# Performance work log

Measured on AMD Instinct MI355X. Metric: run time of the kernel, lower is better.

## Reference

```python
import jax, jax.numpy as jnp
import numpy as np

# Model constants (match init_kwargs)
H, P, N, G, NL, K = 32, 64, 128, 1, 15, 4   # heads, head_dim, state, groups, lambda levels, conv width
HID, T, BATCH = 1024, 1024, 1
INTER = H * P                    # 2048
CONV_DIM = INTER + 2 * G * N     # 2304
PROJ = INTER + CONV_DIM + H * (NL + 1)  # 4864
EPS = 1e-5


def _level_matrix(t_len: int) -> np.ndarray:
    """Fenwick-tree level assignment: for query t, prefix [0,t] splits into
    power-of-two segments from binary expansion of t+1; segment of length 2^l -> level l."""
    lm = np.zeros((t_len, t_len), dtype=np.int32)
    for t in range(t_len):
        n = t + 1
        while n > 0:
            lb = n & (-n)
            lm[t, n - lb:n] = lb.bit_length() - 1
            n -= lb
    return lm


def setup_inputs() -> dict:
    key = jax.random.key(0)
    ks = jax.random.split(key, 4)
    return {
        "hidden_states": jax.random.normal(ks[0], (BATCH, T, HID), jnp.float32),
        "in_proj_w": jax.random.normal(ks[1], (PROJ, HID), jnp.float32) / np.sqrt(HID).astype(np.float32),
        "in_proj_b": jnp.zeros((PROJ,), jnp.float32),
        "conv_w": jax.random.normal(ks[2], (CONV_DIM, K), jnp.float32) / np.sqrt(K).astype(np.float32),
        "dt_bias": jnp.ones((H,), jnp.float32),
        "A_log": jnp.log(jnp.arange(1, H + 1, dtype=jnp.float32)),
        "L_param": jnp.ones((H, NL), jnp.float32),
        "D": jnp.ones((H,), jnp.float32),
        "rmsnorm_w": jnp.ones((INTER,), jnp.float32),
        "out_proj_w": jax.random.normal(ks[3], (HID, INTER), jnp.float32) / np.sqrt(INTER).astype(np.float32),
        "out_proj_b": jnp.zeros((HID,), jnp.float32),
        "level_mat": jnp.asarray(_level_matrix(T)),  # (T,T) int32, data-independent
    }


def reference(hidden_states, in_proj_w, in_proj_b, conv_w, dt_bias, A_log,
              L_param, D, rmsnorm_w, out_proj_w, out_proj_b, level_mat):
    b, t, _ = hidden_states.shape
    # in_proj and split: [z | xBC | dt | dl]
    zxbcdtdl = hidden_states @ in_proj_w.T + in_proj_b
    z, xBC, dt, dl = jnp.split(zxbcdtdl, [INTER, INTER + CONV_DIM, INTER + CONV_DIM + H], axis=-1)
    # depthwise causal conv1d (width K) + SiLU
    xp = jnp.pad(xBC, ((0, 0), (K - 1, 0), (0, 0)))
    conv = sum(xp[:, w:w + t, :] * conv_w[:, w] for w in range(K))
    xBC = jax.nn.silu(conv)
    x, Bm, Cm = jnp.split(xBC, [INTER, INTER + G * N], axis=-1)
    x = x.reshape(b, t, H, P)          # v pre-scale
    Bm = Bm.reshape(b, t, G, N)        # keys
    Cm = Cm.reshape(b, t, G, N)        # queries
    dl = dl.reshape(b, t, H, NL)
    # D residual uses unscaled x (matches hmamba_chunk_scan_combined ordering)
    D_res = x * D[None, None, :, None]
    dt = jax.nn.softplus(dt + dt_bias)            # (b,t,H)
    v = x * dt[..., None]                          # (b,t,H,P)
    A = -jnp.exp(A_log)                            # (H,)
    g = A * dt                                     # (b,t,H), per-token log-decay (<=0)
    Ls = jax.nn.softplus(L_param * dl)             # (b,t,H,NL) per-token level scales
    # cumulative log-decay; decay(t,s) = exp(cg_t - cg_s), s<=t
    cg = jnp.cumsum(g, axis=1).transpose(0, 2, 1)  # (b,H,t)
    mask = jnp.tril(jnp.ones((t, t), bool))
    logdecay = jnp.where(mask, cg[:, :, :, None] - cg[:, :, None, :], -jnp.inf)
    decay = jnp.exp(logdecay)                      # (b,H,t,s)
    # hierarchical level scale H[t,s] = Ls[b,t,h, level(t,s)]
    Hmat = jnp.take_along_axis(Ls.transpose(0, 2, 1, 3), level_mat[None, None, :, :], axis=-1)  # (b,H,t,s)
    scores = jnp.einsum('btgn,bsgn->bgts', Cm, Bm)  # (b,G,t,s), G=1 broadcasts over heads
    att = scores * decay * Hmat                     # (b,H,t,s), masked via decay=0
    y = jnp.einsum('bhts,bshp->bthp', att, v) + D_res
    y = y.reshape(b, t, INTER)
    # gated RMSNorm with norm_before_gate=False: normalize(y * silu(z)) * w
    yg = y * jax.nn.silu(z)
    y = yg * jax.lax.rsqrt(jnp.mean(yg * yg, axis=-1, keepdims=True) + EPS) * rmsnorm_w
    return y @ out_proj_w.T + out_proj_b
```

## Files before the change

kernel.cpp:

```cpp
#include <hip/hip_runtime.h>
#include <hip/hip_bf16.h>
#include <math.h>

#define T_LEN 1024
#define HID 1024
#define NHEAD 32
#define HDIM 64
#define NSTATE 128
#define NLVL 15
#define KCONV 4
#define INTER 2048
#define CONV_DIM 2304
#define PROJ 4864
#define EPS 1e-5f

typedef __attribute__((ext_vector_type(8))) _Float16 half8;
typedef __attribute__((ext_vector_type(4))) float float4v;
typedef unsigned short ushort_t;

__device__ __forceinline__ float softplus_f(float x) {
  return fmaxf(x, 0.f) + log1pf(expf(-fabsf(x)));
}
__device__ __forceinline__ float silu_f(float x) {
  return x / (1.f + expf(-x));
}
__device__ __forceinline__ ushort_t f2h(float f) {
  union { _Float16 h; ushort_t u; } v;
  v.h = (_Float16)f;
  return v.u;
}
__device__ __forceinline__ float h2f(ushort_t u) {
  union { ushort_t u; _Float16 h; } v;
  v.u = u;
  return (float)v.h;
}
__device__ __forceinline__ void gload_lds16(const void* g, void* l) {
  __builtin_amdgcn_global_load_lds(
      (const __attribute__((address_space(1))) void*)g,
      (__attribute__((address_space(3))) void*)l, 16, 0, 0);
}

#define N4_HS  (T_LEN * HID / 4)
#define N4_WI  (PROJ * HID / 4)
#define N4_WO  (HID * INTER / 4)
__global__ __launch_bounds__(256) void prep_f16(
    const float* __restrict__ hs, const float* __restrict__ wi,
    const float* __restrict__ wo, ushort_t* __restrict__ hsb,
    ushort_t* __restrict__ wib, ushort_t* __restrict__ wob) {
  int i = blockIdx.x * 256 + threadIdx.x;
  const float* src; ushort_t* dst; int j;
  if (i < N4_HS)              { src = hs; dst = hsb; j = i; }
  else if (i < N4_HS + N4_WI) { src = wi; dst = wib; j = i - N4_HS; }
  else                        { src = wo; dst = wob; j = i - N4_HS - N4_WI; }
  float4 v = reinterpret_cast<const float4*>(src)[j];
  union { ushort_t u[4]; unsigned long long ll; } o;
  o.u[0] = f2h(v.x); o.u[1] = f2h(v.y); o.u[2] = f2h(v.z); o.u[3] = f2h(v.w);
  reinterpret_cast<unsigned long long*>(dst)[j] = o.ll;
}

__global__ __launch_bounds__(256) void gemm_f16_sk(
    const ushort_t* __restrict__ A, const ushort_t* __restrict__ B,
    ushort_t* __restrict__ Cpart, int M, int N, int K, int Kc) {
  __shared__ ushort_t As[2][128][32];
  __shared__ ushort_t Bs[2][128][32];
  const int tid = threadIdx.x;
  const int w = tid >> 6, L = tid & 63;
  const int n0 = blockIdx.x * 128, m0 = blockIdx.y * 128;
  const int kbeg = blockIdx.z * Kc;
  ushort_t* __restrict__ C = Cpart + (size_t)blockIdx.z * M * N;
  const int mq = (w & 1) * 64, nq = (w >> 1) * 64;
  const int srow = (L >> 2);
  const int sch = (L & 3) * 8;

  float4v acc[4][4];
#pragma unroll
  for (int i = 0; i < 4; ++i)
#pragma unroll
    for (int j = 0; j < 4; ++j) acc[i][j] = (float4v){0.f, 0.f, 0.f, 0.f};

  const int niter = Kc / 32;
  {
    const int kk = kbeg;
#pragma unroll
    for (int j = 0; j < 2; ++j) {
      int r0 = 16 * (w * 2 + j);
      gload_lds16(A + (size_t)(m0 + r0 + srow) * K + kk + sch, &As[0][r0][0]);
      gload_lds16(B + (size_t)(n0 + r0 + srow) * K + kk + sch, &Bs[0][r0][0]);
    }
  }
  for (int it = 0; it < niter; ++it) {
    __syncthreads();
    if (it + 1 < niter) {
      const int kk = kbeg + (it + 1) * 32;
      const int nb = (it + 1) & 1;
#pragma unroll
      for (int j = 0; j < 2; ++j) {
        int r0 = 16 * (w * 2 + j);
        gload_lds16(A + (size_t)(m0 + r0 + srow) * K + kk + sch, &As[nb][r0][0]);
        gload_lds16(B + (size_t)(n0 + r0 + srow) * K + kk + sch, &Bs[nb][r0][0]);
      }
    }
    const int cb = it & 1;
    half8 af[4], bf[4];
#pragma unroll
    for (int t = 0; t < 4; ++t) {
      af[t] = *reinterpret_cast<const half8*>(&As[cb][mq + t * 16 + (L & 15)][(L >> 4) * 8]);
      bf[t] = *reinterpret_cast<const half8*>(&Bs[cb][nq + t * 16 + (L & 15)][(L >> 4) * 8]);
    }
#pragma unroll
    for (int mt = 0; mt < 4; ++mt)
#pragma unroll
      for (int nt = 0; nt < 4; ++nt)
        acc[mt][nt] = __builtin_amdgcn_mfma_f32_16x16x32_f16(af[mt], bf[nt], acc[mt][nt], 0, 0, 0);
  }
  const int qrow = (L >> 4) * 4;
#pragma unroll
  for (int mt = 0; mt < 4; ++mt) {
#pragma unroll
    for (int nt = 0; nt < 4; ++nt) {
      int col = n0 + nq + nt * 16 + (L & 15);
#pragma unroll
      for (int r = 0; r < 4; ++r) {
        int row = m0 + mq + mt * 16 + qrow + r;
        C[(size_t)row * N + col] = f2h(acc[mt][nt][r]);
      }
    }
  }
}

__global__ __launch_bounds__(256) void reduce_out4(const ushort_t* __restrict__ p,
                                                   const float* __restrict__ bias,
                                                   float* __restrict__ out, int MN) {
  int i = blockIdx.x * 256 + threadIdx.x;
  if (i * 8 >= MN) return;
  half8 a = reinterpret_cast<const half8*>(p)[i];
  half8 b = reinterpret_cast<const half8*>(p + MN)[i];
  half8 c = reinterpret_cast<const half8*>(p + 2 * (size_t)MN)[i];
  half8 d = reinterpret_cast<const half8*>(p + 3 * (size_t)MN)[i];
  int col = (i * 8) & (HID - 1);
  float o[8];
#pragma unroll
  for (int j = 0; j < 8; ++j)
    o[j] = (float)a[j] + (float)b[j] + (float)c[j] + (float)d[j] + bias[col + j];
  float4 o0 = {o[0], o[1], o[2], o[3]}, o1 = {o[4], o[5], o[6], o[7]};
  reinterpret_cast<float4*>(out)[i * 2] = o0;
  reinterpret_cast<float4*>(out)[i * 2 + 1] = o1;
}

__global__ __launch_bounds__(64) void scan_g(
    const ushort_t* __restrict__ zh0, const ushort_t* __restrict__ zh1,
    const float* __restrict__ in_b, const float* __restrict__ dt_bias,
    const float* __restrict__ A_log, float* __restrict__ dtb,
    double* __restrict__ cgd) {
  const int h = blockIdx.x, l = threadIdx.x;
  const int c = INTER + CONV_DIM + h;
  const float bb = in_b[c] + dt_bias[h];
  const float Ae = -expf(A_log[h]);
  double pre[16];
  double acc = 0.0;
#pragma unroll
  for (int i = 0; i < 16; ++i) {
    int t = l * 16 + i;
    size_t o = (size_t)t * PROJ + c;
    float x = h2f(zh0[o]) + h2f(zh1[o]) + bb;
    float dt = softplus_f(x);
    dtb[t * NHEAD + h] = dt;
    acc += (double)(Ae * dt);
    pre[i] = acc;
  }
  double s = acc;
#pragma unroll
  for (int off = 1; off < 64; off <<= 1) {
    double o = __shfl_up(s, off, 64);
    if (l >= off) s += o;
  }
  const double base = s - acc;
  double* cr = cgd + (size_t)h * T_LEN + l * 16;
#pragma unroll
  for (int i = 0; i < 16; ++i) cr[i] = base + pre[i];
}

__global__ __launch_bounds__(256) void conv_fused(
    const ushort_t* __restrict__ zh0, const ushort_t* __restrict__ zh1,
    const float* __restrict__ in_b, const float* __restrict__ conv_w,
    const float* __restrict__ dtb, const float* __restrict__ Dp,
    ushort_t* __restrict__ vt, float* __restrict__ ybuf,
    ushort_t* __restrict__ Bb, ushort_t* __restrict__ Cb) {
  __shared__ ushort_t Vl[64][68];
  __shared__ float dtl[64];
  const int tq = blockIdx.x, cy = blockIdx.y;
  const int t0 = tq * 64;
  const int tid = threadIdx.x;
  const int lane = tid & 63, g = tid >> 6;
  const bool vpath = (cy < 32);
  const int ccol = vpath ? cy * 64 + lane : INTER + (cy - 32) * 64 + lane;
  const int zcol = INTER + ccol;
  float cw[KCONV];
#pragma unroll
  for (int w = 0; w < KCONV; ++w) cw[w] = conv_w[ccol * KCONV + w];
  const float bc = in_b[zcol];
  if (vpath && tid < 64) dtl[tid] = dtb[(t0 + tid) * NHEAD + cy];
  const float Dh = vpath ? Dp[cy] : 0.f;

  float xv[19];
#pragma unroll
  for (int i = 0; i < 19; ++i) {
    int tt = t0 + g * 16 - 3 + i;
    if (tt >= 0) {
      size_t o = (size_t)tt * PROJ + zcol;
      xv[i] = h2f(zh0[o]) + h2f(zh1[o]) + bc;
    } else xv[i] = 0.f;
  }
  __syncthreads();
#pragma unroll
  for (int i = 0; i < 16; ++i) {
    float acc = xv[i] * cw[0] + xv[i + 1] * cw[1] + xv[i + 2] * cw[2] + xv[i + 3] * cw[3];
    float sil = silu_f(acc);
    int tl = g * 16 + i;
    int t = t0 + tl;
    if (vpath) {
      Vl[tl][lane] = f2h(sil * dtl[tl]);
      ybuf[(size_t)t * INTER + cy * 64 + lane] = sil * Dh;
    } else if (ccol < INTER + NSTATE) {
      Bb[t * NSTATE + (ccol - INTER)] = f2h(sil);
    } else {
      Cb[t * NSTATE + (ccol - INTER - NSTATE)] = f2h(sil);
    }
  }
  if (vpath) {
    __syncthreads();
#pragma unroll
    for (int rep = 0; rep < 2; ++rep) {
      int u = tid + 256 * rep;
      int p = u >> 3, t8 = (u & 7) * 8;
      union { ushort_t u16[8]; half8 h; } o;
#pragma unroll
      for (int j = 0; j < 8; ++j) o.u16[j] = Vl[t8 + j][p];
      *reinterpret_cast<half8*>(vt + (size_t)(cy * 64 + p) * T_LEN + t0 + t8) = o.h;
    }
  }
}

__global__ __launch_bounds__(256) void attn_mfma(
    const ushort_t* __restrict__ Bb, const ushort_t* __restrict__ Cb,
    const ushort_t* __restrict__ vt, const double* __restrict__ cgd,
    const ushort_t* __restrict__ zh0, const ushort_t* __restrict__ zh1,
    const float* __restrict__ in_b, const float* __restrict__ L_param,
    float* __restrict__ ybuf) {
  __shared__ ushort_t Bl[64][136];
  __shared__ ushort_t Vtl[64][72];
  __shared__ ushort_t Sl[64][72];
  __shared__ float Lsl[64][16];
  __shared__ float cgq[64];
  __shared__ float cgs[64];

  const int item = blockIdx.x;
  const int h = item / 40;
  const int rem = item - h * 40;
  int qt, j;
  if (rem < 4)        { qt = rem;                 j = 0; }
  else if (rem < 12)  { qt = 4 + (rem - 4) / 2;   j = (rem - 4) % 2; }
  else if (rem < 24)  { qt = 8 + (rem - 12) / 3;  j = (rem - 12) % 3; }
  else                { qt = 12 + (rem - 24) / 4; j = (rem - 24) % 4; }

  const int tid = threadIdx.x;
  const int w = tid >> 6, L = tid & 63;
  const int tq0 = qt * 64;
  const double* cgh = cgd + (size_t)h * T_LEN;
  const double base = cgh[tq0];

  for (int i = tid; i < 64 * NLVL; i += 256) {
    int r = i / NLVL, l = i - r * NLVL;
    int cc = INTER + CONV_DIM + NHEAD + h * NLVL + l;
    size_t o = (size_t)(tq0 + r) * PROJ + cc;
    float x = h2f(zh0[o]) + h2f(zh1[o]) + in_b[cc];
    Lsl[r][l] = softplus_f(L_param[h * NLVL + l] * x);
  }
  if (tid < 64) cgq[tid] = (float)(cgh[tq0 + tid] - base);

  half8 cfrag[4];
  {
    const ushort_t* cr = Cb + (size_t)(tq0 + w * 16 + (L & 15)) * NSTATE + (L >> 4) * 8;
#pragma unroll
    for (int ks = 0; ks < 4; ++ks)
      cfrag[ks] = *reinterpret_cast<const half8*>(cr + ks * 32);
  }
  float4v yac[4];
#pragma unroll
  for (int i = 0; i < 4; ++i) yac[i] = (float4v){0.f, 0.f, 0.f, 0.f};

  const int qrow = w * 16 + ((L >> 4) << 2);

  const int st0 = 4 * j;
  const int st1 = min(4 * j + 4, qt + 1);
  for (int st = st0; st < st1; ++st) {
    const int ts0 = st * 64;
    __syncthreads();
#pragma unroll
    for (int i = 0; i < 4; ++i) {
      int u = tid + 256 * i;
      int row = u >> 4, kb = (u & 15) * 8;
      *reinterpret_cast<half8*>(&Bl[row][kb]) =
          *reinterpret_cast<const half8*>(Bb + (size_t)(ts0 + row) * NSTATE + kb);
    }
#pragma unroll
    for (int i = 0; i < 2; ++i) {
      int u = tid + 256 * i;
      int p = u >> 3, sc = (u & 7) * 8;
      *reinterpret_cast<half8*>(&Vtl[p][sc]) =
          *reinterpret_cast<const half8*>(vt + (size_t)(h * HDIM + p) * T_LEN + ts0 + sc);
    }
    if (tid < 64) cgs[tid] = (float)(cgh[ts0 + tid] - base);
    __syncthreads();

    float4v sac[4];
#pragma unroll
    for (int nt = 0; nt < 4; ++nt) sac[nt] = (float4v){0.f, 0.f, 0.f, 0.f};
#pragma unroll
    for (int ks = 0; ks < 4; ++ks) {
#pragma unroll
      for (int nt = 0; nt < 4; ++nt) {
        half8 bfrag = *reinterpret_cast<const half8*>(&Bl[nt * 16 + (L & 15)][ks * 32 + (L >> 4) * 8]);
        sac[nt] = __builtin_amdgcn_mfma_f32_16x16x32_f16(cfrag[ks], bfrag, sac[nt], 0, 0, 0);
      }
    }
#pragma unroll
    for (int nt = 0; nt < 4; ++nt) {
      int s = nt * 16 + (L & 15);
      int sg = ts0 + s;
      float cs = cgs[s];
#pragma unroll
      for (int r = 0; r < 4; ++r) {
        int q = qrow + r;
        int tg = tq0 + q;
        float val = 0.f;
        if (sg <= tg) {
          int lvl = 31 - __clz((unsigned)(sg ^ (tg + 1)));
          val = sac[nt][r] * __expf(cgq[q] - cs) * Lsl[q][lvl];
        }
        Sl[q][s] = f2h(val);
      }
    }
    __builtin_amdgcn_s_waitcnt(0xC07F);
#pragma unroll
    for (int ks = 0; ks < 2; ++ks) {
      half8 af = *reinterpret_cast<const half8*>(&Sl[w * 16 + (L & 15)][ks * 32 + (L >> 4) * 8]);
#pragma unroll
      for (int pt = 0; pt < 4; ++pt) {
        half8 bfv = *reinterpret_cast<const half8*>(&Vtl[pt * 16 + (L & 15)][ks * 32 + (L >> 4) * 8]);
        yac[pt] = __builtin_amdgcn_mfma_f32_16x16x32_f16(af, bfv, yac[pt], 0, 0, 0);
      }
    }
  }
#pragma unroll
  for (int pt = 0; pt < 4; ++pt) {
    int p = pt * 16 + (L & 15);
#pragma unroll
    for (int r = 0; r < 4; ++r) {
      int q = qrow + r;
      atomicAdd(ybuf + (size_t)(tq0 + q) * INTER + h * HDIM + p, yac[pt][r]);
    }
  }
}

__global__ __launch_bounds__(256) void rmsnorm_gate(
    const float* __restrict__ ybuf, const ushort_t* __restrict__ zh0,
    const ushort_t* __restrict__ zh1, const float* __restrict__ in_b,
    const float* __restrict__ w, ushort_t* __restrict__ yhf) {
  __shared__ float red[4];
  const int t = blockIdx.x, tid = threadIdx.x;
  const size_t ro = (size_t)t * PROJ;
  const float* yrow = ybuf + (size_t)t * INTER;
  float yg[8];
  float ss = 0.f;
#pragma unroll
  for (int i = 0; i < 8; ++i) {
    int c = tid + 256 * i;
    float z = h2f(zh0[ro + c]) + h2f(zh1[ro + c]) + in_b[c];
    float g = yrow[c] * silu_f(z);
    yg[i] = g;
    ss += g * g;
  }
#pragma unroll
  for (int off = 32; off; off >>= 1) ss += __shfl_down(ss, off, 64);
  if ((tid & 63) == 0) red[tid >> 6] = ss;
  __syncthreads();
  if (tid == 0) red[0] = red[0] + red[1] + red[2] + red[3];
  __syncthreads();
  const float scale = rsqrtf(red[0] / (float)INTER + EPS);
#pragma unroll
  for (int i = 0; i < 8; ++i) {
    int c = tid + 256 * i;
    yhf[(size_t)t * INTER + c] = f2h(yg[i] * scale * w[c]);
  }
}

extern "C" void kernel_launch(void* const* d_in, const int* in_sizes, int n_in,
                              void* d_out, int out_size, void* d_ws, size_t ws_size,
                              hipStream_t stream) {
  const float* hs        = (const float*)d_in[0];
  const float* in_proj_w = (const float*)d_in[1];
  const float* in_proj_b = (const float*)d_in[2];
  const float* conv_w    = (const float*)d_in[3];
  const float* dt_bias   = (const float*)d_in[4];
  const float* A_log     = (const float*)d_in[5];
  const float* L_param   = (const float*)d_in[6];
  const float* Dp        = (const float*)d_in[7];
  const float* rms_w     = (const float*)d_in[8];
  const float* out_proj_w= (const float*)d_in[9];
  const float* out_proj_b= (const float*)d_in[10];
  float* out = (float*)d_out;

  char* W = (char*)d_ws;
  size_t off = 0;
  auto alloc = [&](size_t bytes) { void* p = W + off; off = (off + bytes + 255) & ~(size_t)255; return p; };
  double*   cgd = (double*)  alloc((size_t)NHEAD * T_LEN * 8);
  ushort_t* zh  = (ushort_t*)alloc((size_t)2 * T_LEN * PROJ * 2);
  ushort_t* opp = (ushort_t*)alloc((size_t)4 * T_LEN * HID * 2);
  float*    ybuf= (float*)   alloc((size_t)T_LEN * INTER * 4);
  float*    dtb = (float*)   alloc((size_t)T_LEN * NHEAD * 4);
  ushort_t* hsb = (ushort_t*)alloc((size_t)T_LEN * HID * 2);
  ushort_t* Wib = (ushort_t*)alloc((size_t)PROJ * HID * 2);
  ushort_t* Wob = (ushort_t*)alloc((size_t)HID * INTER * 2);
  ushort_t* yhf = (ushort_t*)alloc((size_t)T_LEN * INTER * 2);
  ushort_t* vt  = (ushort_t*)alloc((size_t)T_LEN * INTER * 2);
  ushort_t* Bb  = (ushort_t*)alloc((size_t)T_LEN * NSTATE * 2);
  ushort_t* Cb  = (ushort_t*)alloc((size_t)T_LEN * NSTATE * 2);
  ushort_t* zh0 = zh;
  ushort_t* zh1 = zh + (size_t)T_LEN * PROJ;

  prep_f16<<<(N4_HS + N4_WI + N4_WO) / 256, 256, 0, stream>>>(
      hs, in_proj_w, out_proj_w, hsb, Wib, Wob);

  gemm_f16_sk<<<dim3(PROJ / 128, T_LEN / 128, 2), 256, 0, stream>>>(
      hsb, Wib, zh, T_LEN, PROJ, HID, HID / 2);

  scan_g<<<NHEAD, 64, 0, stream>>>(zh0, zh1, in_proj_b, dt_bias, A_log, dtb, cgd);

  conv_fused<<<dim3(T_LEN / 64, 36), 256, 0, stream>>>(
      zh0, zh1, in_proj_b, conv_w, dtb, Dp, vt, ybuf, Bb, Cb);

  attn_mfma<<<NHEAD * 40, 256, 0, stream>>>(Bb, Cb, vt, cgd, zh0, zh1, in_proj_b,
                                            L_param, ybuf);

  rmsnorm_gate<<<T_LEN, 256, 0, stream>>>(ybuf, zh0, zh1, in_proj_b, rms_w, yhf);

  gemm_f16_sk<<<dim3(HID / 128, T_LEN / 128, 4), 256, 0, stream>>>(
      yhf, Wob, opp, T_LEN, HID, INTER, INTER / 4);
  reduce_out4<<<(T_LEN * HID / 8 + 255) / 256, 256, 0, stream>>>(
      opp, out_proj_b, out, T_LEN * HID);
}
```

Before: 200.7 us.

## Raise split-K factors for both GEMMs and vectorize consumer loads of partials

Increases split-K from 2 to 4 for the input projection and from 4 to 8 for the output projection, so more workgroups are launched on the many CUs. All consumers (scan, conv, attention level scales, rmsnorm) now sum four fp16 partials. The conv kernel stages its input window through shared memory with 8-wide vector loads, and rmsnorm switches to contiguous half8 and float4 loads and stores. The cost is extra partial-buffer traffic and more fp16 rounding from the additional partial sums.

```diff
diff --git a/kernel.cpp b/kernel.cpp
--- a/kernel.cpp
+++ b/kernel.cpp
@@ -13,6 +13,7 @@
 #define CONV_DIM 2304
 #define PROJ 4864
 #define EPS 1e-5f
+#define TPROJ ((size_t)T_LEN * PROJ)
 
 typedef __attribute__((ext_vector_type(8))) _Float16 half8;
 typedef __attribute__((ext_vector_type(4))) float float4v;
@@ -128,30 +129,30 @@
   }
 }
 
-__global__ __launch_bounds__(256) void reduce_out4(const ushort_t* __restrict__ p,
+__global__ __launch_bounds__(256) void reduce_out8(const ushort_t* __restrict__ p,
                                                    const float* __restrict__ bias,
                                                    float* __restrict__ out, int MN) {
   int i = blockIdx.x * 256 + threadIdx.x;
   if (i * 8 >= MN) return;
-  half8 a = reinterpret_cast<const half8*>(p)[i];
-  half8 b = reinterpret_cast<const half8*>(p + MN)[i];
-  half8 c = reinterpret_cast<const half8*>(p + 2 * (size_t)MN)[i];
-  half8 d = reinterpret_cast<const half8*>(p + 3 * (size_t)MN)[i];
+  float o[8] = {0.f, 0.f, 0.f, 0.f, 0.f, 0.f, 0.f, 0.f};
+#pragma unroll
+  for (int z = 0; z < 8; ++z) {
+    half8 v = reinterpret_cast<const half8*>(p + (size_t)z * MN)[i];
+#pragma unroll
+    for (int j = 0; j < 8; ++j) o[j] += (float)v[j];
+  }
   int col = (i * 8) & (HID - 1);
-  float o[8];
-#pragma unroll
-  for (int j = 0; j < 8; ++j)
-    o[j] = (float)a[j] + (float)b[j] + (float)c[j] + (float)d[j] + bias[col + j];
+#pragma unroll
+  for (int j = 0; j < 8; ++j) o[j] += bias[col + j];
   float4 o0 = {o[0], o[1], o[2], o[3]}, o1 = {o[4], o[5], o[6], o[7]};
   reinterpret_cast<float4*>(out)[i * 2] = o0;
   reinterpret_cast<float4*>(out)[i * 2 + 1] = o1;
 }
 
 __global__ __launch_bounds__(64) void scan_g(
-    const ushort_t* __restrict__ zh0, const ushort_t* __restrict__ zh1,
-    const float* __restrict__ in_b, const float* __restrict__ dt_bias,
-    const float* __restrict__ A_log, float* __restrict__ dtb,
-    double* __restrict__ cgd) {
+    const ushort_t* __restrict__ zh, const float* __restrict__ in_b,
+    const float* __restrict__ dt_bias, const float* __restrict__ A_log,
+    float* __restrict__ dtb, double* __restrict__ cgd) {
   const int h = blockIdx.x, l = threadIdx.x;
   const int c = INTER + CONV_DIM + h;
   const float bb = in_b[c] + dt_bias[h];
@@ -162,7 +163,8 @@
   for (int i = 0; i < 16; ++i) {
     int t = l * 16 + i;
     size_t o = (size_t)t * PROJ + c;
-    float x = h2f(zh0[o]) + h2f(zh1[o]) + bb;
+    float x = h2f(zh[o]) + h2f(zh[TPROJ + o]) + h2f(zh[2 * TPROJ + o]) +
+              h2f(zh[3 * TPROJ + o]) + bb;
     float dt = softplus_f(x);
     dtb[t * NHEAD + h] = dt;
     acc += (double)(Ae * dt);
@@ -181,11 +183,12 @@
 }
 
 __global__ __launch_bounds__(256) void conv_fused(
-    const ushort_t* __restrict__ zh0, const ushort_t* __restrict__ zh1,
-    const float* __restrict__ in_b, const float* __restrict__ conv_w,
-    const float* __restrict__ dtb, const float* __restrict__ Dp,
-    ushort_t* __restrict__ vt, float* __restrict__ ybuf,
-    ushort_t* __restrict__ Bb, ushort_t* __restrict__ Cb) {
+    const ushort_t* __restrict__ zh, const float* __restrict__ in_b,
+    const float* __restrict__ conv_w, const float* __restrict__ dtb,
+    const float* __restrict__ Dp, ushort_t* __restrict__ vt,
+    float* __restrict__ ybuf, ushort_t* __restrict__ Bb,
+    ushort_t* __restrict__ Cb) {
+  __shared__ float Xl[67][68];
   __shared__ ushort_t Vl[64][68];
   __shared__ float dtl[64];
   const int tq = blockIdx.x, cy = blockIdx.y;
@@ -193,34 +196,47 @@
   const int tid = threadIdx.x;
   const int lane = tid & 63, g = tid >> 6;
   const bool vpath = (cy < 32);
-  const int ccol = vpath ? cy * 64 + lane : INTER + (cy - 32) * 64 + lane;
-  const int zcol = INTER + ccol;
-  float cw[KCONV];
-#pragma unroll
-  for (int w = 0; w < KCONV; ++w) cw[w] = conv_w[ccol * KCONV + w];
-  const float bc = in_b[zcol];
+  const int c0 = vpath ? cy * 64 : INTER + (cy - 32) * 64;
   if (vpath && tid < 64) dtl[tid] = dtb[(t0 + tid) * NHEAD + cy];
+
+  for (int u = tid; u < 67 * 8; u += 256) {
+    int r = u >> 3, c8 = (u & 7) * 8;
+    int t = t0 - 3 + r;
+    float xs[8];
+    if (t >= 0) {
+      size_t o = (size_t)t * PROJ + INTER + c0 + c8;
+      half8 a = *reinterpret_cast<const half8*>(zh + o);
+      half8 b = *reinterpret_cast<const half8*>(zh + TPROJ + o);
+      half8 c = *reinterpret_cast<const half8*>(zh + 2 * TPROJ + o);
+      half8 d = *reinterpret_cast<const half8*>(zh + 3 * TPROJ + o);
+#pragma unroll
+      for (int j = 0; j < 8; ++j)
+        xs[j] = (float)a[j] + (float)b[j] + (float)c[j] + (float)d[j] +
+                in_b[INTER + c0 + c8 + j];
+    } else {
+#pragma unroll
+      for (int j = 0; j < 8; ++j) xs[j] = 0.f;
+    }
+#pragma unroll
+    for (int j = 0; j < 8; ++j) Xl[r][c8 + j] = xs[j];
+  }
+  __syncthreads();
+
+  const int ccol = c0 + lane;
+  const float4 cwv = *reinterpret_cast<const float4*>(conv_w + ccol * KCONV);
   const float Dh = vpath ? Dp[cy] : 0.f;
-
   float xv[19];
 #pragma unroll
-  for (int i = 0; i < 19; ++i) {
-    int tt = t0 + g * 16 - 3 + i;
-    if (tt >= 0) {
-      size_t o = (size_t)tt * PROJ + zcol;
-      xv[i] = h2f(zh0[o]) + h2f(zh1[o]) + bc;
-    } else xv[i] = 0.f;
-  }
-  __syncthreads();
+  for (int i = 0; i < 19; ++i) xv[i] = Xl[g * 16 + i][lane];
 #pragma unroll
   for (int i = 0; i < 16; ++i) {
-    float acc = xv[i] * cw[0] + xv[i + 1] * cw[1] + xv[i + 2] * cw[2] + xv[i + 3] * cw[3];
+    float acc = xv[i] * cwv.x + xv[i + 1] * cwv.y + xv[i + 2] * cwv.z + xv[i + 3] * cwv.w;
     float sil = silu_f(acc);
     int tl = g * 16 + i;
     int t = t0 + tl;
     if (vpath) {
       Vl[tl][lane] = f2h(sil * dtl[tl]);
-      ybuf[(size_t)t * INTER + cy * 64 + lane] = sil * Dh;
+      ybuf[(size_t)t * INTER + c0 + lane] = sil * Dh;
     } else if (ccol < INTER + NSTATE) {
       Bb[t * NSTATE + (ccol - INTER)] = f2h(sil);
     } else {
@@ -236,7 +252,7 @@
       union { ushort_t u16[8]; half8 h; } o;
 #pragma unroll
       for (int j = 0; j < 8; ++j) o.u16[j] = Vl[t8 + j][p];
-      *reinterpret_cast<half8*>(vt + (size_t)(cy * 64 + p) * T_LEN + t0 + t8) = o.h;
+      *reinterpret_cast<half8*>(vt + (size_t)(c0 + p) * T_LEN + t0 + t8) = o.h;
     }
   }
 }
@@ -244,9 +260,8 @@
 __global__ __launch_bounds__(256) void attn_mfma(
     const ushort_t* __restrict__ Bb, const ushort_t* __restrict__ Cb,
     const ushort_t* __restrict__ vt, const double* __restrict__ cgd,
-    const ushort_t* __restrict__ zh0, const ushort_t* __restrict__ zh1,
-    const float* __restrict__ in_b, const float* __restrict__ L_param,
-    float* __restrict__ ybuf) {
+    const ushort_t* __restrict__ zh, const float* __restrict__ in_b,
+    const float* __restrict__ L_param, float* __restrict__ ybuf) {
   __shared__ ushort_t Bl[64][136];
   __shared__ ushort_t Vtl[64][72];
   __shared__ ushort_t Sl[64][72];
@@ -273,7 +288,8 @@
     int r = i / NLVL, l = i - r * NLVL;
     int cc = INTER + CONV_DIM + NHEAD + h * NLVL + l;
     size_t o = (size_t)(tq0 + r) * PROJ + cc;
-    float x = h2f(zh0[o]) + h2f(zh1[o]) + in_b[cc];
+    float x = h2f(zh[o]) + h2f(zh[TPROJ + o]) + h2f(zh[2 * TPROJ + o]) +
+              h2f(zh[3 * TPROJ + o]) + in_b[cc];
     Lsl[r][l] = softplus_f(L_param[h * NLVL + l] * x);
   }
   if (tid < 64) cgq[tid] = (float)(cgh[tq0 + tid] - base);
@@ -364,21 +380,27 @@
 }
 
 __global__ __launch_bounds__(256) void rmsnorm_gate(
-    const float* __restrict__ ybuf, const ushort_t* __restrict__ zh0,
-    const ushort_t* __restrict__ zh1, const float* __restrict__ in_b,
-    const float* __restrict__ w, ushort_t* __restrict__ yhf) {
+    const float* __restrict__ ybuf, const ushort_t* __restrict__ zh,
+    const float* __restrict__ in_b, const float* __restrict__ w,
+    ushort_t* __restrict__ yhf) {
   __shared__ float red[4];
   const int t = blockIdx.x, tid = threadIdx.x;
-  const size_t ro = (size_t)t * PROJ;
-  const float* yrow = ybuf + (size_t)t * INTER;
+  const size_t ro = (size_t)t * PROJ + tid * 8;
+  const float* yrow = ybuf + (size_t)t * INTER + tid * 8;
+  half8 a = *reinterpret_cast<const half8*>(zh + ro);
+  half8 b = *reinterpret_cast<const half8*>(zh + TPROJ + ro);
+  half8 c = *reinterpret_cast<const half8*>(zh + 2 * TPROJ + ro);
+  half8 d = *reinterpret_cast<const half8*>(zh + 3 * TPROJ + ro);
+  float4 y0 = reinterpret_cast<const float4*>(yrow)[0];
+  float4 y1 = reinterpret_cast<const float4*>(yrow)[1];
+  float yv[8] = {y0.x, y0.y, y0.z, y0.w, y1.x, y1.y, y1.z, y1.w};
   float yg[8];
   float ss = 0.f;
 #pragma unroll
-  for (int i = 0; i < 8; ++i) {
-    int c = tid + 256 * i;
-    float z = h2f(zh0[ro + c]) + h2f(zh1[ro + c]) + in_b[c];
-    float g = yrow[c] * silu_f(z);
-    yg[i] = g;
+  for (int j = 0; j < 8; ++j) {
+    float z = (float)a[j] + (float)b[j] + (float)c[j] + (float)d[j] + in_b[tid * 8 + j];
+    float g = yv[j] * silu_f(z);
+    yg[j] = g;
     ss += g * g;
   }
 #pragma unroll
@@ -388,11 +410,10 @@
   if (tid == 0) red[0] = red[0] + red[1] + red[2] + red[3];
   __syncthreads();
   const float scale = rsqrtf(red[0] / (float)INTER + EPS);
-#pragma unroll
-  for (int i = 0; i < 8; ++i) {
-    int c = tid + 256 * i;
-    yhf[(size_t)t * INTER + c] = f2h(yg[i] * scale * w[c]);
-  }
+  union { ushort_t u[8]; half8 h; } o;
+#pragma unroll
+  for (int j = 0; j < 8; ++j) o.u[j] = f2h(yg[j] * scale * w[tid * 8 + j]);
+  *reinterpret_cast<half8*>(yhf + (size_t)t * INTER + tid * 8) = o.h;
 }
 
 extern "C" void kernel_launch(void* const* d_in, const int* in_sizes, int n_in,
@@ -415,8 +436,8 @@
   size_t off = 0;
   auto alloc = [&](size_t bytes) { void* p = W + off; off = (off + bytes + 255) & ~(size_t)255; return p; };
   double*   cgd = (double*)  alloc((size_t)NHEAD * T_LEN * 8);
-  ushort_t* zh  = (ushort_t*)alloc((size_t)2 * T_LEN * PROJ * 2);
-  ushort_t* opp = (ushort_t*)alloc((size_t)4 * T_LEN * HID * 2);
+  ushort_t* zh  = (ushort_t*)alloc((size_t)4 * TPROJ * 2);
+  ushort_t* opp = (ushort_t*)alloc((size_t)8 * T_LEN * HID * 2);
   float*    ybuf= (float*)   alloc((size_t)T_LEN * INTER * 4);
   float*    dtb = (float*)   alloc((size_t)T_LEN * NHEAD * 4);
   ushort_t* hsb = (ushort_t*)alloc((size_t)T_LEN * HID * 2);
@@ -426,27 +447,25 @@
   ushort_t* vt  = (ushort_t*)alloc((size_t)T_LEN * INTER * 2);
   ushort_t* Bb  = (ushort_t*)alloc((size_t)T_LEN * NSTATE * 2);
   ushort_t* Cb  = (ushort_t*)alloc((size_t)T_LEN * NSTATE * 2);
-  ushort_t* zh0 = zh;
-  ushort_t* zh1 = zh + (size_t)T_LEN * PROJ;
 
   prep_f16<<<(N4_HS + N4_WI + N4_WO) / 256, 256, 0, stream>>>(
       hs, in_proj_w, out_proj_w, hsb, Wib, Wob);
 
-  gemm_f16_sk<<<dim3(PROJ / 128, T_LEN / 128, 2), 256, 0, stream>>>(
-      hsb, Wib, zh, T_LEN, PROJ, HID, HID / 2);
-
-  scan_g<<<NHEAD, 64, 0, stream>>>(zh0, zh1, in_proj_b, dt_bias, A_log, dtb, cgd);
+  gemm_f16_sk<<<dim3(PROJ / 128, T_LEN / 128, 4), 256, 0, stream>>>(
+      hsb, Wib, zh, T_LEN, PROJ, HID, HID / 4);
+
+  scan_g<<<NHEAD, 64, 0, stream>>>(zh, in_proj_b, dt_bias, A_log, dtb, cgd);
 
   conv_fused<<<dim3(T_LEN / 64, 36), 256, 0, stream>>>(
-      zh0, zh1, in_proj_b, conv_w, dtb, Dp, vt, ybuf, Bb, Cb);
-
-  attn_mfma<<<NHEAD * 40, 256, 0, stream>>>(Bb, Cb, vt, cgd, zh0, zh1, in_proj_b,
+      zh, in_proj_b, conv_w, dtb, Dp, vt, ybuf, Bb, Cb);
+
+  attn_mfma<<<NHEAD * 40, 256, 0, stream>>>(Bb, Cb, vt, cgd, zh, in_proj_b,
                                             L_param, ybuf);
 
-  rmsnorm_gate<<<T_LEN, 256, 0, stream>>>(ybuf, zh0, zh1, in_proj_b, rms_w, yhf);
-
-  gemm_f16_sk<<<dim3(HID / 128, T_LEN / 128, 4), 256, 0, stream>>>(
-      yhf, Wob, opp, T_LEN, HID, INTER, INTER / 4);
-  reduce_out4<<<(T_LEN * HID / 8 + 255) / 256, 256, 0, stream>>>(
+  rmsnorm_gate<<<T_LEN, 256, 0, stream>>>(ybuf, zh, in_proj_b, rms_w, yhf);
+
+  gemm_f16_sk<<<dim3(HID / 128, T_LEN / 128, 8), 256, 0, stream>>>(
+      yhf, Wob, opp, T_LEN, HID, INTER, INTER / 8);
+  reduce_out8<<<(T_LEN * HID / 8 + 255) / 256, 256, 0, stream>>>(
       opp, out_proj_b, out, T_LEN * HID);
 }
```

Result: no change. 201.9 us (+0.6%).
